# Optimization experiments

Hardware: AMD Instinct MI355X
Metric: run time of the kernel (lower is better)

## Reference

```python
import jax, jax.numpy as jnp
import numpy as np

B, SQ, SK, D = 8, 2048, 2048, 256

def setup_inputs() -> dict:
    key = jax.random.key(0)
    ks = jax.random.split(key, 8)
    x1 = jax.random.normal(ks[0], (B, SQ, D), dtype=jnp.float32)
    x2 = jax.random.normal(ks[1], (B, SK, D), dtype=jnp.float32)
    x3 = jax.random.normal(ks[2], (B, SK, D), dtype=jnp.float32)  # unused by the original forward (value=x3 is dead)
    mask = jax.random.bernoulli(ks[3], 0.8, (B, SK))
    scale = 0.02
    Wq = jax.random.normal(ks[4], (D, D), dtype=jnp.float32) * scale
    Wk = jax.random.normal(ks[5], (D, D), dtype=jnp.float32) * scale
    Wv = jax.random.normal(ks[6], (D, D), dtype=jnp.float32) * scale
    bq = jnp.zeros((D,), jnp.float32)
    bk = jnp.zeros((D,), jnp.float32)
    bv = jnp.zeros((D,), jnp.float32)
    return {"x1": x1, "x2": x2, "x3": x3, "Wq": Wq, "Wk": Wk, "Wv": Wv,
            "bq": bq, "bk": bk, "bv": bv, "mask": mask}

def reference(x1, x2, x3, Wq, Wk, Wv, bq, bk, bv, mask):
    d = x1.shape[-1]
    inv_sqrt_d = 1.0 / jnp.sqrt(jnp.asarray(d, x1.dtype))
    # Projections (single-head MHA with query scaling, as in torch MHA internals)
    q = (x1 @ Wq + bq) * inv_sqrt_d          # [B, SQ, D]
    k = x2 @ Wk + bk                          # [B, SK, D]
    v = x2 @ Wv + bv                          # forward_value(key): value projected from key input
    # Raw scores
    qk = jnp.einsum('bqd,bkd->bqk', q, k)     # [B, SQ, SK]
    # Mask-derived per-column rescale: qk /= (mask.size(0)/mask.sum(-2))**0.5
    m = mask.astype(qk.dtype)                 # [B, SK]
    col_count = jnp.sum(m, axis=0, keepdims=True)           # [1, SK]
    factor = jnp.sqrt(jnp.asarray(mask.shape[0], qk.dtype) / col_count)  # [1, SK]
    qk = qk / factor                          # broadcast over [B, SQ, SK]; div-by-inf -> 0 where column count is 0
    attn = jax.nn.softmax(qk, axis=-1)
    # dropout is identity in eval / p=0
    out = jnp.einsum('bqk,bkd->bqd', attn, v)  # [B, SQ, D]
    return out
```

## Files before the change

kernel.cpp:

```cpp
#include <hip/hip_runtime.h>
#include <hip/hip_bf16.h>
#include <math.h>

#define B_  8
#define SQ_ 2048
#define SK_ 2048
#define D_  256
#define NSPLIT 4
#define KEYS_PER_SPLIT (SK_ / NSPLIT)
#define NT (KEYS_PER_SPLIT / 32)

typedef __attribute__((ext_vector_type(8))) short bf16x8;
typedef __attribute__((ext_vector_type(4))) float f32x4;
typedef __attribute__((ext_vector_type(4))) unsigned short u16x4;
typedef __attribute__((ext_vector_type(8))) _Float16 f16x8;

static __device__ __forceinline__ unsigned short f2bf(float f) {
    unsigned int u = __builtin_bit_cast(unsigned int, f);
    u += 0x7FFFu + ((u >> 16) & 1u);
    return (unsigned short)(u >> 16);
}

static __device__ __forceinline__ void gld_lds16(const unsigned short* g, unsigned short* l) {
    __builtin_amdgcn_global_load_lds(
        (const __attribute__((address_space(1))) unsigned int*)g,
        (__attribute__((address_space(3))) unsigned int*)l, 16, 0, 0);
}

__global__ void prep_kernel(const float* __restrict__ Wq, const float* __restrict__ Wk,
                            const float* __restrict__ Wv, const int* __restrict__ mask,
                            unsigned short* __restrict__ wP, float* __restrict__ r) {
    int bid = blockIdx.x, tid = threadIdx.x;
    if (bid < 24) {
        int p = bid >> 3, c = bid & 7;
        const float* W = (p == 0 ? Wq : (p == 1 ? Wk : Wv));
#pragma unroll
        for (int it = 0; it < 4; it++) {
            int chunk = it * 256 + tid;
            int nt = chunk >> 6, lane = chunk & 63;
            int l15 = lane & 15, quad = lane >> 4;
            int n = nt * 16 + l15;
            unsigned short* dst = wP + (size_t)(((p * 8 + c) * 16 + nt) * 1024 + lane * 8);
#pragma unroll
            for (int j = 0; j < 8; j++)
                dst[j] = f2bf(W[(size_t)(c * 32 + quad * 8 + j) * D_ + n]);
        }
    } else {
        int s = (bid - 24) * 256 + tid;
        float c = 0.f;
#pragma unroll
        for (int b = 0; b < B_; b++) c += (mask[b * SK_ + s] != 0) ? 1.f : 0.f;
        r[s] = sqrtf(c * 0.125f);
    }
}

__global__ __launch_bounds__(256) void proj_kernel(
    const float* __restrict__ x1, const float* __restrict__ x2,
    const float* __restrict__ bq, const float* __restrict__ bk, const float* __restrict__ bv,
    const unsigned short* __restrict__ wP, const float* __restrict__ r,
    unsigned short* __restrict__ qb, unsigned short* __restrict__ kb,
    unsigned short* __restrict__ vt)
{
    __shared__ unsigned short sbuf[18432];
    const int tid = threadIdx.x;
    const int wv = tid >> 6, lane = tid & 63, l15 = lane & 15, quad = lane >> 4;
    const int mt = blockIdx.x, b = blockIdx.y, p = blockIdx.z;
    const int s0w = mt * 64 + wv * 16;

    const float* x = (p == 0 ? x1 : x2) + ((size_t)b * SQ_ + s0w + l15) * D_;
    const unsigned short* wbase = wP + (size_t)(p * 8) * 16 * 1024;
    const float* bias = (p == 0 ? bq : (p == 1 ? bk : bv));

    float4 xa[8], xb[8];
#pragma unroll
    for (int c = 0; c < 8; c++) {
        xa[c] = *(const float4*)(x + c * 32 + quad * 8);
        xb[c] = *(const float4*)(x + c * 32 + quad * 8 + 4);
    }
    bf16x8 af[8];
#pragma unroll
    for (int c = 0; c < 8; c++) {
        bf16x8 t;
        t[0] = (short)f2bf(xa[c].x); t[1] = (short)f2bf(xa[c].y);
        t[2] = (short)f2bf(xa[c].z); t[3] = (short)f2bf(xa[c].w);
        t[4] = (short)f2bf(xb[c].x); t[5] = (short)f2bf(xb[c].y);
        t[6] = (short)f2bf(xb[c].z); t[7] = (short)f2bf(xb[c].w);
        af[c] = t;
    }

    float bb[16];
#pragma unroll
    for (int nt = 0; nt < 16; nt++) bb[nt] = bias[nt * 16 + l15];

    f32x4 acc[16];
#pragma unroll
    for (int n = 0; n < 16; n++) acc[n] = (f32x4){0.f, 0.f, 0.f, 0.f};

#pragma unroll
    for (int c = 0; c < 8; c++) {
        const unsigned short* wc = wbase + (size_t)c * 16 * 1024 + lane * 8;
#pragma unroll
        for (int nt = 0; nt < 16; nt++) {
            bf16x8 wf = *(const bf16x8*)(wc + nt * 1024);
            acc[nt] = __builtin_amdgcn_mfma_f32_16x16x32_bf16(af[c], wf, acc[nt], 0, 0, 0);
        }
    }

    if (p == 2) {
#pragma unroll
        for (int nt = 0; nt < 16; nt++) {
            int d = nt * 16 + l15;
            u16x4 u;
#pragma unroll
            for (int g = 0; g < 4; g++) u[g] = f2bf(acc[nt][g] + bb[nt]);
            *(u16x4*)(sbuf + (size_t)d * 72 + wv * 16 + quad * 4) = u;
        }
        __syncthreads();
#pragma unroll
        for (int it = 0; it < 8; it++) {
            int chunk = it * 256 + tid;
            int d = chunk >> 3, s8 = chunk & 7;
            bf16x8 v = *(const bf16x8*)(sbuf + (size_t)d * 72 + s8 * 8);
            *(bf16x8*)(vt + ((size_t)b * D_ + d) * SK_ + mt * 64 + s8 * 8) = v;
        }
    } else {
        unsigned short* dst = (p == 0 ? qb : kb);
        float rv[4];
#pragma unroll
        for (int g = 0; g < 4; g++)
            rv[g] = (p == 1) ? r[s0w + quad * 4 + g] : 0.0625f;
        unsigned short* my = sbuf + wv * 2176;
#pragma unroll
        for (int h = 0; h < 2; h++) {
#pragma unroll
            for (int nt8 = 0; nt8 < 8; nt8++) {
                int nt = h * 8 + nt8;
#pragma unroll
                for (int g = 0; g < 4; g++) {
                    float v = (acc[nt][g] + bb[nt]) * rv[g];
                    my[(quad * 4 + g) * 136 + nt8 * 16 + l15] = f2bf(v);
                }
            }
            asm volatile("s_waitcnt lgkmcnt(0)" ::: "memory");
#pragma unroll
            for (int i2 = 0; i2 < 4; i2++) {
                int row = i2 * 4 + quad;
                bf16x8 v = *(const bf16x8*)(my + row * 136 + l15 * 8);
                *(bf16x8*)(dst + ((size_t)b * SQ_ + s0w + row) * D_ + h * 128 + l15 * 8) = v;
            }
        }
    }
}

__global__ __launch_bounds__(256, 2) void flash_kernel(
    const unsigned short* __restrict__ qb, const unsigned short* __restrict__ kb,
    const unsigned short* __restrict__ vt, _Float16* __restrict__ Op,
    float* __restrict__ lp)
{
    __shared__ unsigned short Ks[2][32 * 256];
    __shared__ unsigned short Vs[2][256 * 32];
    __shared__ unsigned short Ps[4][32][40];
    const int tid = threadIdx.x;
    const int wv = tid >> 6, lane = tid & 63, l15 = lane & 15, quad = lane >> 4;
    const int bid = blockIdx.x;
    const int g = bid & 31, q = bid >> 5;
    const int b = g >> 2, sp = g & 3;
    const int q0 = q * 128 + wv * 32;

    const unsigned short* kbb = kb + ((size_t)b * SK_ + sp * KEYS_PER_SPLIT) * D_;
    const unsigned short* vtb = vt + (size_t)b * D_ * SK_ + sp * KEYS_PER_SPLIT;

    int krow[4], kck[4], vd[4], vch[4];
#pragma unroll
    for (int i = 0; i < 4; i++) {
        int id = i * 256 + tid;
        krow[i] = id >> 5; kck[i] = (id & 31) ^ (krow[i] & 7);
        vd[i] = id >> 2;   vch[i] = (id & 3) ^ ((vd[i] >> 1) & 3);
    }

#pragma unroll
    for (int i = 0; i < 4; i++)
        gld_lds16(kbb + (size_t)krow[i] * D_ + kck[i] * 8, &Ks[0][(i * 256 + wv * 64) * 8]);
#pragma unroll
    for (int i = 0; i < 4; i++)
        gld_lds16(vtb + (size_t)vd[i] * SK_ + vch[i] * 8, &Vs[0][(i * 256 + wv * 64) * 8]);

    bf16x8 qf[2][8];
#pragma unroll
    for (int mt = 0; mt < 2; mt++) {
        const unsigned short* qrow = qb + ((size_t)(b * SQ_ + q0 + mt * 16 + l15)) * D_;
#pragma unroll
        for (int c = 0; c < 8; c++)
            qf[mt][c] = *(const bf16x8*)(qrow + c * 32 + quad * 8);
    }

    f32x4 o[2][16];
#pragma unroll
    for (int mt = 0; mt < 2; mt++)
#pragma unroll
        for (int n = 0; n < 16; n++) o[mt][n] = (f32x4){0.f, 0.f, 0.f, 0.f};
    float l_[2][4] = {{0.f, 0.f, 0.f, 0.f}, {0.f, 0.f, 0.f, 0.f}};

    for (int kt = 0; kt < NT; kt++) {
        const int cur = kt & 1;
        __syncthreads();
        if (kt + 1 < NT) {
            const unsigned short* kn = kbb + (size_t)(kt + 1) * 32 * D_;
            const unsigned short* vn = vtb + (size_t)(kt + 1) * 32;
#pragma unroll
            for (int i = 0; i < 4; i++)
                gld_lds16(kn + (size_t)krow[i] * D_ + kck[i] * 8,
                          &Ks[cur ^ 1][(i * 256 + wv * 64) * 8]);
#pragma unroll
            for (int i = 0; i < 4; i++)
                gld_lds16(vn + (size_t)vd[i] * SK_ + vch[i] * 8,
                          &Vs[cur ^ 1][(i * 256 + wv * 64) * 8]);
        }

        f32x4 s[2][2];
        s[0][0] = (f32x4){0.f,0.f,0.f,0.f}; s[0][1] = (f32x4){0.f,0.f,0.f,0.f};
        s[1][0] = (f32x4){0.f,0.f,0.f,0.f}; s[1][1] = (f32x4){0.f,0.f,0.f,0.f};
#pragma unroll
        for (int h = 0; h < 2; h++)
#pragma unroll
            for (int c = 0; c < 8; c++) {
                bf16x8 kf = *(const bf16x8*)(
                    &Ks[cur][(h * 16 + l15) * 256 + (((c * 4 + quad) ^ (l15 & 7)) * 8)]);
                s[0][h] = __builtin_amdgcn_mfma_f32_16x16x32_bf16(qf[0][c], kf, s[0][h], 0, 0, 0);
                s[1][h] = __builtin_amdgcn_mfma_f32_16x16x32_bf16(qf[1][c], kf, s[1][h], 0, 0, 0);
            }

#pragma unroll
        for (int mt = 0; mt < 2; mt++)
#pragma unroll
            for (int h = 0; h < 2; h++)
#pragma unroll
                for (int g2 = 0; g2 < 4; g2++) {
                    float pv = __expf(s[mt][h][g2]);
                    l_[mt][g2] += pv;
                    Ps[wv][mt * 16 + quad * 4 + g2][h * 16 + l15] = f2bf(pv);
                }
        asm volatile("s_waitcnt lgkmcnt(0)" ::: "memory");

        bf16x8 pf0 = *(const bf16x8*)(&Ps[wv][l15][quad * 8]);
        bf16x8 pf1 = *(const bf16x8*)(&Ps[wv][16 + l15][quad * 8]);

        const int vsw = ((quad ^ ((l15 >> 1) & 3)) * 8);
#pragma unroll
        for (int n = 0; n < 16; n++) {
            bf16x8 vf = *(const bf16x8*)(&Vs[cur][(n * 16 + l15) * 32 + vsw]);
            o[0][n] = __builtin_amdgcn_mfma_f32_16x16x32_bf16(pf0, vf, o[0][n], 0, 0, 0);
            o[1][n] = __builtin_amdgcn_mfma_f32_16x16x32_bf16(pf1, vf, o[1][n], 0, 0, 0);
        }
    }

#pragma unroll
    for (int mt = 0; mt < 2; mt++)
#pragma unroll
        for (int g2 = 0; g2 < 4; g2++) {
            float t = l_[mt][g2];
            t += __shfl_xor(t, 1, 64);
            t += __shfl_xor(t, 2, 64);
            t += __shfl_xor(t, 4, 64);
            t += __shfl_xor(t, 8, 64);
            l_[mt][g2] = t;
        }

    _Float16* op = Op + ((size_t)(sp * B_ + b) * SQ_ + q0) * D_;
#pragma unroll
    for (int mt = 0; mt < 2; mt++)
#pragma unroll
        for (int g2 = 0; g2 < 4; g2++) {
            size_t ro = (size_t)(mt * 16 + quad * 4 + g2) * D_ + l15;
#pragma unroll
            for (int n = 0; n < 16; n++)
                op[ro + n * 16] = (_Float16)(o[mt][n][g2]);
        }
    if (l15 == 0) {
        float* lpp = lp + (size_t)(sp * B_ + b) * SQ_ + q0;
#pragma unroll
        for (int mt = 0; mt < 2; mt++)
#pragma unroll
            for (int g2 = 0; g2 < 4; g2++)
                lpp[mt * 16 + quad * 4 + g2] = l_[mt][g2];
    }
}

__global__ __launch_bounds__(256) void combine_kernel(
    const _Float16* __restrict__ Op, const float* __restrict__ lp,
    float* __restrict__ out)
{
    const int gid = blockIdx.x * 256 + threadIdx.x;
    const int row = gid >> 5;
    const size_t base = (size_t)gid * 8;
    float l = lp[row] + lp[B_ * SQ_ + row] + lp[2 * B_ * SQ_ + row] + lp[3 * B_ * SQ_ + row];
    float inv = 1.f / l;
    float acc[8] = {0,0,0,0,0,0,0,0};
#pragma unroll
    for (int sp = 0; sp < NSPLIT; sp++) {
        f16x8 v = *(const f16x8*)(Op + (size_t)sp * B_ * SQ_ * D_ + base);
#pragma unroll
        for (int j = 0; j < 8; j++) acc[j] += (float)v[j];
    }
    float4 r0 = {acc[0] * inv, acc[1] * inv, acc[2] * inv, acc[3] * inv};
    float4 r1 = {acc[4] * inv, acc[5] * inv, acc[6] * inv, acc[7] * inv};
    *(float4*)(out + base) = r0;
    *(float4*)(out + base + 4) = r1;
}

extern "C" void kernel_launch(void* const* d_in, const int* in_sizes, int n_in,
                              void* d_out, int out_size, void* d_ws, size_t ws_size,
                              hipStream_t stream)
{
    const float* x1 = (const float*)d_in[0];
    const float* x2 = (const float*)d_in[1];
    const float* Wq = (const float*)d_in[3];
    const float* Wk = (const float*)d_in[4];
    const float* Wv = (const float*)d_in[5];
    const float* bq = (const float*)d_in[6];
    const float* bk = (const float*)d_in[7];
    const float* bv = (const float*)d_in[8];
    const int*  mask = (const int*)d_in[9];
    float* out = (float*)d_out;

    char* ws = (char*)d_ws;
    unsigned short* qb = (unsigned short*)(ws);
    unsigned short* kb = (unsigned short*)(ws + 8388608);
    unsigned short* vt = (unsigned short*)(ws + 16777216);
    float*          r  = (float*)(ws + 25165824);
    float*          lp = (float*)(ws + 25174016);
    _Float16*       Op = (_Float16*)(ws + 25436160);
    unsigned short* wP = (unsigned short*)(ws + 25436160);

    prep_kernel<<<dim3(24 + SK_ / 256), 256, 0, stream>>>(Wq, Wk, Wv, mask, wP, r);
    proj_kernel<<<dim3(SQ_ / 64, B_, 3), 256, 0, stream>>>(x1, x2, bq, bk, bv, wP, r, qb, kb, vt);
    flash_kernel<<<dim3((SQ_ / 128) * B_ * NSPLIT), 256, 0, stream>>>(qb, kb, vt, Op, lp);
    combine_kernel<<<dim3((B_ * SQ_ * D_ / 8) / 256), 256, 0, stream>>>(Op, lp, out);
}
```

Measured before the change: 186.5 us.

## Transpose MFMA operands to keep P in registers and drop LDS staging

Swaps the A/B operands of both MFMAs so score tiles come out transposed, letting the exp'd probabilities be packed to bf16 with v_cvt_pk_bf16_f32 and rearranged with permlane swaps directly into the PV operand layout, removing the per-tile LDS write/read of P and its wait. Row sums become per-lane accumulations reduced across quads, and output stores become vectorized f16x4 writes. It also adds s_setprio around the MFMA blocks to favor matrix issue across waves. This relies on gfx950-specific permlane instructions and on the lane mapping being exactly right.

```diff
diff --git a/kernel.cpp b/kernel.cpp
--- a/kernel.cpp
+++ b/kernel.cpp
@@ -14,6 +14,8 @@
 typedef __attribute__((ext_vector_type(4))) float f32x4;
 typedef __attribute__((ext_vector_type(4))) unsigned short u16x4;
 typedef __attribute__((ext_vector_type(8))) _Float16 f16x8;
+typedef __attribute__((ext_vector_type(4))) _Float16 f16x4;
+typedef __attribute__((ext_vector_type(4))) unsigned int u32x4;
 
 static __device__ __forceinline__ unsigned short f2bf(float f) {
     unsigned int u = __builtin_bit_cast(unsigned int, f);
@@ -159,7 +161,6 @@
 {
     __shared__ unsigned short Ks[2][32 * 256];
     __shared__ unsigned short Vs[2][256 * 32];
-    __shared__ unsigned short Ps[4][32][40];
     const int tid = threadIdx.x;
     const int wv = tid >> 6, lane = tid & 63, l15 = lane & 15, quad = lane >> 4;
     const int bid = blockIdx.x;
@@ -199,7 +200,9 @@
     for (int mt = 0; mt < 2; mt++)
 #pragma unroll
         for (int n = 0; n < 16; n++) o[mt][n] = (f32x4){0.f, 0.f, 0.f, 0.f};
-    float l_[2][4] = {{0.f, 0.f, 0.f, 0.f}, {0.f, 0.f, 0.f, 0.f}};
+    float l_[2] = {0.f, 0.f};
+
+    const int vsw = ((quad ^ ((l15 >> 1) & 3)) * 8);
 
     for (int kt = 0; kt < NT; kt++) {
         const int cur = kt & 1;
@@ -220,69 +223,73 @@
         f32x4 s[2][2];
         s[0][0] = (f32x4){0.f,0.f,0.f,0.f}; s[0][1] = (f32x4){0.f,0.f,0.f,0.f};
         s[1][0] = (f32x4){0.f,0.f,0.f,0.f}; s[1][1] = (f32x4){0.f,0.f,0.f,0.f};
+        __builtin_amdgcn_s_setprio(1);
 #pragma unroll
         for (int h = 0; h < 2; h++)
 #pragma unroll
             for (int c = 0; c < 8; c++) {
                 bf16x8 kf = *(const bf16x8*)(
                     &Ks[cur][(h * 16 + l15) * 256 + (((c * 4 + quad) ^ (l15 & 7)) * 8)]);
-                s[0][h] = __builtin_amdgcn_mfma_f32_16x16x32_bf16(qf[0][c], kf, s[0][h], 0, 0, 0);
-                s[1][h] = __builtin_amdgcn_mfma_f32_16x16x32_bf16(qf[1][c], kf, s[1][h], 0, 0, 0);
+                s[0][h] = __builtin_amdgcn_mfma_f32_16x16x32_bf16(kf, qf[0][c], s[0][h], 0, 0, 0);
+                s[1][h] = __builtin_amdgcn_mfma_f32_16x16x32_bf16(kf, qf[1][c], s[1][h], 0, 0, 0);
             }
-
-#pragma unroll
-        for (int mt = 0; mt < 2; mt++)
-#pragma unroll
-            for (int h = 0; h < 2; h++)
-#pragma unroll
-                for (int g2 = 0; g2 < 4; g2++) {
-                    float pv = __expf(s[mt][h][g2]);
-                    l_[mt][g2] += pv;
-                    Ps[wv][mt * 16 + quad * 4 + g2][h * 16 + l15] = f2bf(pv);
-                }
-        asm volatile("s_waitcnt lgkmcnt(0)" ::: "memory");
-
-        bf16x8 pf0 = *(const bf16x8*)(&Ps[wv][l15][quad * 8]);
-        bf16x8 pf1 = *(const bf16x8*)(&Ps[wv][16 + l15][quad * 8]);
-
-        const int vsw = ((quad ^ ((l15 >> 1) & 3)) * 8);
+        __builtin_amdgcn_s_setprio(0);
+
+        bf16x8 pf[2];
+#pragma unroll
+        for (int mt = 0; mt < 2; mt++) {
+            float e0 = __expf(s[mt][0][0]), e1 = __expf(s[mt][0][1]);
+            float e2 = __expf(s[mt][0][2]), e3 = __expf(s[mt][0][3]);
+            float f0 = __expf(s[mt][1][0]), f1 = __expf(s[mt][1][1]);
+            float f2 = __expf(s[mt][1][2]), f3 = __expf(s[mt][1][3]);
+            l_[mt] += (e0 + e1 + e2 + e3) + (f0 + f1 + f2 + f3);
+            unsigned int pk0, pk1, pk2, pk3;
+            asm("v_cvt_pk_bf16_f32 %0, %1, %2" : "=v"(pk0) : "v"(e0), "v"(e1));
+            asm("v_cvt_pk_bf16_f32 %0, %1, %2" : "=v"(pk1) : "v"(e2), "v"(e3));
+            asm("v_cvt_pk_bf16_f32 %0, %1, %2" : "=v"(pk2) : "v"(f0), "v"(f1));
+            asm("v_cvt_pk_bf16_f32 %0, %1, %2" : "=v"(pk3) : "v"(f2), "v"(f3));
+            asm("v_permlane32_swap_b32 %0, %1" : "+v"(pk0), "+v"(pk2));
+            asm("v_permlane16_swap_b32 %0, %1" : "+v"(pk0), "+v"(pk2));
+            asm("v_permlane32_swap_b32 %0, %1" : "+v"(pk1), "+v"(pk3));
+            asm("v_permlane16_swap_b32 %0, %1" : "+v"(pk1), "+v"(pk3));
+            u32x4 w = (u32x4){pk0, pk1, pk2, pk3};
+            pf[mt] = __builtin_bit_cast(bf16x8, w);
+        }
+
+        __builtin_amdgcn_s_setprio(1);
 #pragma unroll
         for (int n = 0; n < 16; n++) {
             bf16x8 vf = *(const bf16x8*)(&Vs[cur][(n * 16 + l15) * 32 + vsw]);
-            o[0][n] = __builtin_amdgcn_mfma_f32_16x16x32_bf16(pf0, vf, o[0][n], 0, 0, 0);
-            o[1][n] = __builtin_amdgcn_mfma_f32_16x16x32_bf16(pf1, vf, o[1][n], 0, 0, 0);
-        }
-    }
-
-#pragma unroll
-    for (int mt = 0; mt < 2; mt++)
-#pragma unroll
-        for (int g2 = 0; g2 < 4; g2++) {
-            float t = l_[mt][g2];
-            t += __shfl_xor(t, 1, 64);
-            t += __shfl_xor(t, 2, 64);
-            t += __shfl_xor(t, 4, 64);
-            t += __shfl_xor(t, 8, 64);
-            l_[mt][g2] = t;
-        }
+            o[0][n] = __builtin_amdgcn_mfma_f32_16x16x32_bf16(vf, pf[0], o[0][n], 0, 0, 0);
+            o[1][n] = __builtin_amdgcn_mfma_f32_16x16x32_bf16(vf, pf[1], o[1][n], 0, 0, 0);
+        }
+        __builtin_amdgcn_s_setprio(0);
+    }
+
+#pragma unroll
+    for (int mt = 0; mt < 2; mt++) {
+        float t = l_[mt];
+        t += __shfl_xor(t, 16, 64);
+        t += __shfl_xor(t, 32, 64);
+        l_[mt] = t;
+    }
 
     _Float16* op = Op + ((size_t)(sp * B_ + b) * SQ_ + q0) * D_;
 #pragma unroll
-    for (int mt = 0; mt < 2; mt++)
-#pragma unroll
-        for (int g2 = 0; g2 < 4; g2++) {
-            size_t ro = (size_t)(mt * 16 + quad * 4 + g2) * D_ + l15;
-#pragma unroll
-            for (int n = 0; n < 16; n++)
-                op[ro + n * 16] = (_Float16)(o[mt][n][g2]);
-        }
-    if (l15 == 0) {
+    for (int mt = 0; mt < 2; mt++) {
+        _Float16* rowp = op + (size_t)(mt * 16 + l15) * D_ + quad * 4;
+#pragma unroll
+        for (int n = 0; n < 16; n++) {
+            f16x4 v4;
+#pragma unroll
+            for (int g2 = 0; g2 < 4; g2++) v4[g2] = (_Float16)(o[mt][n][g2]);
+            *(f16x4*)(rowp + n * 16) = v4;
+        }
+    }
+    if (quad == 0) {
         float* lpp = lp + (size_t)(sp * B_ + b) * SQ_ + q0;
-#pragma unroll
-        for (int mt = 0; mt < 2; mt++)
-#pragma unroll
-            for (int g2 = 0; g2 < 4; g2++)
-                lpp[mt * 16 + quad * 4 + g2] = l_[mt][g2];
+        lpp[l15] = l_[0];
+        lpp[16 + l15] = l_[1];
     }
 }
 
```

Result: faster. 180.6 us (-3.2%).
